# Kernel optimization log

Hardware: AMD Instinct MI355X
Metric: run time of the kernel (lower is better)

Reference implementation:

```python
import jax, jax.numpy as jnp
import numpy as np

C, FF, NH = 128, 2048, 8
B, D, H, W = 1, 16, 16, 16
EPS = 1e-5

def setup_inputs() -> dict:
    key = jax.random.key(0)
    ks = jax.random.split(key, 20)
    s = 0.02
    inp = {
        'x': jax.random.normal(ks[0], (B, C, D, H, W), jnp.float32),
        'Wq': jax.random.normal(ks[1], (C, C), jnp.float32) * s,
        'bq': jnp.zeros((C,), jnp.float32),
        'Wk': jax.random.normal(ks[2], (C, C), jnp.float32) * s,
        'bk': jnp.zeros((C,), jnp.float32),
        'Wv': jax.random.normal(ks[3], (C, C), jnp.float32) * s,
        'bv': jnp.zeros((C,), jnp.float32),
        'Wo': jax.random.normal(ks[4], (C, C), jnp.float32) * s,
        'bo': jnp.zeros((C,), jnp.float32),
        'W1': jax.random.normal(ks[5], (FF, C), jnp.float32) * s,
        'b1': jnp.zeros((FF,), jnp.float32),
        'W2': jax.random.normal(ks[6], (C, FF), jnp.float32) * s,
        'b2': jnp.zeros((C,), jnp.float32),
        'g1': jnp.ones((C,), jnp.float32),
        'be1': jnp.zeros((C,), jnp.float32),
        'g2': jnp.ones((C,), jnp.float32),
        'be2': jnp.zeros((C,), jnp.float32),
    }
    return inp

def _layernorm(t, g, b):
    # normalize over last (channel) dim, biased variance like torch LayerNorm
    m = jnp.mean(t, axis=-1, keepdims=True)
    v = jnp.mean(jnp.square(t - m), axis=-1, keepdims=True)
    return (t - m) * jax.lax.rsqrt(v + EPS) * g + b

def reference(x, Wq, bq, Wk, bk, Wv, bv, Wo, bo, W1, b1, W2, b2, g1, be1, g2, be2):
    b_, c, d, h, w = x.shape
    n = d * h * w
    hd = c // NH
    xf = x.reshape(b_, c, n)  # [B,C,N]
    # 1x1 conv3d == per-voxel linear over channels
    q = jnp.einsum('oc,bcn->bon', Wq, xf) + bq[:, None]
    k = jnp.einsum('oc,bcn->bon', Wk, xf) + bk[:, None]
    v = jnp.einsum('oc,bcn->bon', Wv, xf) + bv[:, None]
    q = q.reshape(b_, NH, hd, n)
    k = k.reshape(b_, NH, hd, n)
    v = v.reshape(b_, NH, hd, n)
    scores = jnp.einsum('bhcd,bhce->bhde', q, k) / (hd ** 0.5)  # [B,NH,N,N]
    probs = jax.nn.softmax(scores, axis=-1)
    attn = jnp.einsum('bhde,bhce->bhcd', probs, v).reshape(b_, c, n)
    attn = jnp.einsum('oc,bcn->bon', Wo, attn) + bo[:, None]
    x1 = xf + attn  # residual (dropout = identity at eval)
    x1 = _layernorm(x1.transpose(0, 2, 1), g1, be1)  # [B,N,C]
    hmid = jax.nn.relu(jnp.einsum('fc,bnc->bnf', W1, x1) + b1)
    ffn = jnp.einsum('cf,bnf->bnc', W2, hmid) + b2
    x2 = _layernorm(x1 + ffn, g2, be2)
    return x2.transpose(0, 2, 1).reshape(b_, c, d, h, w)
```

## Files before the change

### kernel.cpp

```cpp
#include <hip/hip_runtime.h>
#include <hip/hip_bf16.h>

typedef __hip_bfloat16 bf16;
typedef short short8 __attribute__((ext_vector_type(8)));
typedef float f32x4 __attribute__((ext_vector_type(4)));
typedef unsigned int u32x4 __attribute__((ext_vector_type(4)));

#define C_   128
#define N_   4096
#define NH_  8
#define HD_  16
#define FF_  2048
#define SCALE_Q 0.360673760222241f

__device__ __forceinline__ unsigned short f2bf_bits(float f) {
    bf16 h = __float2bfloat16(f);
    return *reinterpret_cast<unsigned short*>(&h);
}
__device__ __forceinline__ unsigned int pack_trunc(float lo, float hi) {
    return __builtin_amdgcn_perm(__float_as_uint(hi), __float_as_uint(lo), 0x07060302u);
}
__device__ __forceinline__ short f2bf_trunc(float f) {
    return (short)(__float_as_uint(f) >> 16);
}
__device__ __forceinline__ float bfs2f(short s) {
    return __uint_as_float(((unsigned int)(unsigned short)s) << 16);
}
__device__ __forceinline__ float fast_exp2(float x) {
    return __builtin_amdgcn_exp2f(x);
}
__device__ __forceinline__ f32x4 mfma16(short8 a, short8 b, f32x4 c) {
    return __builtin_amdgcn_mfma_f32_16x16x32_bf16(a, b, c, 0, 0, 0);
}

__global__ void __launch_bounds__(256) k_prep(
    const float* __restrict__ Wq, const float* __restrict__ Wk,
    const float* __restrict__ Wv, const float* __restrict__ Wo,
    const float* __restrict__ W1, const float* __restrict__ W2,
    const float* __restrict__ x,
    bf16* __restrict__ Wqkvf, bf16* __restrict__ Wof,
    bf16* __restrict__ W1f, bf16* __restrict__ W2f,
    bf16* __restrict__ xTf)
{
    const int i = blockIdx.x * 256 + threadIdx.x;
    if (i < 73728) {
        const float* row;
        bf16* dst;
        int kblk, g;
        if (i < 8192) {
            const int o = i >> 4;
            kblk = (i >> 2) & 3; g = i & 3;
            const int odx = (o < 384) ? o : o - 384;
            row = (o < 128) ? (Wq + o * 128)
                : (o < 256) ? (Wk + (o - 128) * 128)
                : (o < 384) ? (Wv + (o - 256) * 128)
                            : (Wo + (o - 384) * 128);
            bf16* buf = (o < 384) ? Wqkvf : Wof;
            dst = buf + ((((odx >> 4) << 2) + kblk) * 512 + ((g << 4) + (odx & 15)) * 8);
        } else if (i < 40960) {
            const int t = i - 8192, o = t >> 4;
            kblk = (t >> 2) & 3; g = t & 3;
            row = W1 + o * 128;
            dst = W1f + ((((o >> 4) << 2) + kblk) * 512 + ((g << 4) + (o & 15)) * 8);
        } else {
            const int t = i - 40960, o = t >> 8;
            kblk = (t >> 2) & 63; g = t & 3;
            row = W2 + o * 2048;
            dst = W2f + ((((o >> 4) << 6) + kblk) * 512 + ((g << 4) + (o & 15)) * 8);
        }
        const int k0 = kblk * 32 + g * 4;
        const f32x4 lo = *(const f32x4*)(row + k0);
        const f32x4 hi = *(const f32x4*)(row + k0 + 16);
        u32x4 w;
        #pragma unroll
        for (int j = 0; j < 4; ++j)
            w[j] = ((unsigned int)f2bf_bits(hi[j]) << 16) | f2bf_bits(lo[j]);
        *(u32x4*)dst = w;
    } else {
        const int t = i - 73728;
        const int n = t & 4095, g = (t >> 12) & 3, cblk = t >> 14;
        const int c0 = cblk * 32 + g * 4;
        const float* xs = x + (size_t)c0 * 4096 + n;
        u32x4 w;
        #pragma unroll
        for (int j = 0; j < 4; ++j)
            w[j] = ((unsigned int)f2bf_bits(xs[(size_t)(16 + j) * 4096]) << 16)
                 | f2bf_bits(xs[(size_t)j * 4096]);
        bf16* dst = xTf + ((((n >> 4) << 2) + cblk) * 512 + ((g << 4) + (n & 15)) * 8);
        *(u32x4*)dst = w;
    }
}

__global__ void __launch_bounds__(256) k_qkv(
    const bf16* __restrict__ xTf, const bf16* __restrict__ Wqkvf,
    const float* __restrict__ bq, const float* __restrict__ bk, const float* __restrict__ bv,
    bf16* __restrict__ qf, bf16* __restrict__ kf, bf16* __restrict__ vf)
{
    const int tid = threadIdx.x, wave = tid >> 6, lane = tid & 63;
    const int col = lane & 15, quad = lane >> 4;
    const int gw = blockIdx.x * 4 + wave;
    const int rt = gw / 24, ct = gw % 24;
    f32x4 acc = {};
    #pragma unroll
    for (int c = 0; c < 4; ++c) {
        short8 a = *(const short8*)(xTf + ((size_t)(rt * 4 + c) << 9) + lane * 8);
        short8 b = *(const short8*)(Wqkvf + ((size_t)(ct * 4 + c) << 9) + lane * 8);
        acc = mfma16(a, b, acc);
    }
    #pragma unroll
    for (int r = 0; r < 4; ++r) {
        const int m = rt * 16 + quad * 4 + r;
        const int n = ct * 16 + col;
        const float v = acc[r];
        if (n < 128) {
            const int h = n >> 4, ch = n & 15;
            qf[((h << 8) + (m >> 4)) * 256 + (((ch >> 3) << 4) + (m & 15)) * 8 + (ch & 7)] =
                __float2bfloat16((v + bq[n]) * SCALE_Q);
        } else if (n < 256) {
            const int c2 = n - 128, h = c2 >> 4, ch = c2 & 15;
            kf[((h << 8) + (m >> 4)) * 256 + (((ch >> 3) << 4) + (m & 15)) * 8 + (ch & 7)] =
                __float2bfloat16(v + bk[c2]);
        } else {
            const int c2 = n - 256, h = c2 >> 4, ch = c2 & 15;
            const int ko = m & 31;
            const int pos = ((ko & 15) << 1) + (ko >> 4);
            vf[((h << 7) + (m >> 5)) * 512 + (((pos >> 3) << 4) + ch) * 8 + (pos & 7)] =
                __float2bfloat16(v + bv[c2]);
        }
    }
}

__global__ void __launch_bounds__(256)
attn_kernel(const bf16* __restrict__ qf, const bf16* __restrict__ kf,
            const bf16* __restrict__ vf, bf16* __restrict__ af)
{
    __shared__ __align__(16) union {
        unsigned int P[4][2][320];
        float comb[4][64][8];
    } sh;
    const int tid = threadIdx.x, wave = tid >> 6, lane = tid & 63;
    const int col = lane & 15, quad = lane >> 4;
    const int gw = blockIdx.x;
    const int h  = gw >> 8;
    const int tile = gw & 255;
    const f32x4 zero = {};

    short8 aq = {};
    if (quad < 2)
        aq = *(const short8*)(qf + ((size_t)((h << 8) + tile) << 8) + lane * 8);

    const short8 onesb = { (short)0x3F80, (short)0x3F80, (short)0x3F80, (short)0x3F80,
                           (short)0x3F80, (short)0x3F80, (short)0x3F80, (short)0x3F80 };

    f32x4 accO0 = {}, accO1 = {}, accLa = {}, accLb = {};

    const int kbeg = wave << 10;
    unsigned int* P0 = &sh.P[wave][0][0];
    unsigned int* P1 = &sh.P[wave][1][0];

    for (int i = 0; i < 32; i += 2) {
        const int mA = kbeg + (i << 5);
        const int mB = mA + 32;

        short8 bkA0 = {}, bkA1 = {}, bkB0 = {}, bkB1 = {};
        if (quad < 2) {
            const bf16* ka = kf + ((size_t)((h << 8) + (mA >> 4)) << 8) + lane * 8;
            bkA0 = *(const short8*)(ka);
            bkA1 = *(const short8*)(ka + 256);
            bkB0 = *(const short8*)(ka + 512);
            bkB1 = *(const short8*)(ka + 768);
        }
        f32x4 s0 = mfma16(aq, bkA0, zero);
        f32x4 s1 = mfma16(aq, bkA1, zero);
        f32x4 s2 = mfma16(aq, bkB0, zero);
        f32x4 s3 = mfma16(aq, bkB1, zero);
        #pragma unroll
        for (int r = 0; r < 4; ++r) {
            P0[(quad * 4 + r) * 20 + col] = pack_trunc(fast_exp2(s0[r]), fast_exp2(s1[r]));
            P1[(quad * 4 + r) * 20 + col] = pack_trunc(fast_exp2(s2[r]), fast_exp2(s3[r]));
        }
        short8 vA = *(const short8*)(vf + ((size_t)((h << 7) + (mA >> 5)) << 9) + lane * 8);
        short8 vB = *(const short8*)(vf + ((size_t)((h << 7) + (mB >> 5)) << 9) + lane * 8);
        short8 ap0 = *(const short8*)((const short*)P0 + col * 40 + quad * 8);
        accO0 = mfma16(ap0, vA, accO0);
        accLa = mfma16(ap0, onesb, accLa);
        short8 ap1 = *(const short8*)((const short*)P1 + col * 40 + quad * 8);
        accO1 = mfma16(ap1, vB, accO1);
        accLb = mfma16(ap1, onesb, accLb);
    }

    f32x4 accO, accL;
    #pragma unroll
    for (int r = 0; r < 4; ++r) {
        accO[r] = accO0[r] + accO1[r];
        accL[r] = accLa[r] + accLb[r];
    }

    __syncthreads();
    #pragma unroll
    for (int r = 0; r < 4; ++r) {
        sh.comb[wave][lane][r]     = accO[r];
        sh.comb[wave][lane][4 + r] = accL[r];
    }
    __syncthreads();

    if (wave == 0) {
        #pragma unroll
        for (int r = 0; r < 4; ++r) {
            float O = sh.comb[0][lane][r] + sh.comb[1][lane][r]
                    + sh.comb[2][lane][r] + sh.comb[3][lane][r];
            float l = sh.comb[0][lane][4+r] + sh.comb[1][lane][4+r]
                    + sh.comb[2][lane][4+r] + sh.comb[3][lane][4+r];
            const int row16 = quad * 4 + r;
            const int pk = (col << 1) + (h & 1);
            af[((tile << 2) + (h >> 1)) * 512 + (((pk >> 3) << 4) + row16) * 8 + (pk & 7)] =
                __float2bfloat16(O / l);
        }
    }
}

__global__ void __launch_bounds__(512, 2)
k_mega(const bf16* __restrict__ af, const bf16* __restrict__ xTf,
       const bf16* __restrict__ Wof, const bf16* __restrict__ W1f, const bf16* __restrict__ W2f,
       const float* __restrict__ bo, const float* __restrict__ b1, const float* __restrict__ b2,
       const float* __restrict__ g1, const float* __restrict__ be1,
       const float* __restrict__ g2, const float* __restrict__ be2,
       float* __restrict__ out)
{
    __shared__ __align__(16) unsigned int Pb[8][2][320];
    __shared__ float comb[224][64];
    const int tid = threadIdx.x, wave = tid >> 6, lane = tid & 63;
    const int col = lane & 15, quad = lane >> 4;
    const int rt = blockIdx.x, n0 = rt << 4;
    const f32x4 zero = {};

    short8 ao[4], xt[4];
    #pragma unroll
    for (int c = 0; c < 4; ++c) {
        ao[c] = *(const short8*)(af  + ((size_t)(rt * 4 + c) << 9) + lane * 8);
        xt[c] = *(const short8*)(xTf + ((size_t)(rt * 4 + c) << 9) + lane * 8);
    }
    f32x4 d[8];
    #pragma unroll
    for (int t = 0; t < 8; ++t) d[t] = zero;
    #pragma unroll
    for (int t = 0; t < 8; ++t)
        #pragma unroll
        for (int c = 0; c < 4; ++c) {
            short8 b = *(const short8*)(Wof + ((size_t)(t * 4 + c) << 9) + lane * 8);
            d[t] = mfma16(ao[c], b, d[t]);
        }
    #pragma unroll
    for (int t = 0; t < 8; ++t) {
        const float bt = bo[t * 16 + col];
        #pragma unroll
        for (int r = 0; r < 4; ++r) d[t][r] += bt;
    }

    float x1f[4][8];
    #pragma unroll
    for (int c = 0; c < 4; ++c) {
        unsigned int* Pw = &Pb[wave][c & 1][0];
        const short* Ps = (const short*)Pw;
        #pragma unroll
        for (int r = 0; r < 4; ++r)
            Pw[(quad * 4 + r) * 20 + col] = pack_trunc(d[2 * c][r], d[2 * c + 1][r]);
        short8 ar = *(const short8*)(Ps + col * 40 + quad * 8);
        #pragma unroll
        for (int j = 0; j < 8; ++j)
            x1f[c][j] = bfs2f(ar[j]) + bfs2f(xt[c][j]);
    }

    float s = 0.f, ss = 0.f;
    #pragma unroll
    for (int c = 0; c < 4; ++c)
        #pragma unroll
        for (int j = 0; j < 8; ++j) { s += x1f[c][j]; ss += x1f[c][j] * x1f[c][j]; }
    s  += __shfl_xor(s, 16);  s  += __shfl_xor(s, 32);
    ss += __shfl_xor(ss, 16); ss += __shfl_xor(ss, 32);
    const float m1 = s * (1.f / 128.f);
    const float rstd1 = rsqrtf(ss * (1.f / 128.f) - m1 * m1 + 1e-5f);
    short8 aq1[4];
    #pragma unroll
    for (int c = 0; c < 4; ++c)
        #pragma unroll
        for (int j = 0; j < 8; ++j) {
            const int pos = quad * 8 + j;
            const int ko = ((pos & 1) << 4) + (pos >> 1);
            const int ch = c * 32 + ko;
            aq1[c][j] = f2bf_trunc((x1f[c][j] - m1) * rstd1 * g1[ch] + be1[ch]);
        }

    f32x4 ACC[8];
    #pragma unroll
    for (int t = 0; t < 8; ++t) ACC[t] = zero;
    for (int i = 0; i < 8; ++i) {
        const int ffc = (wave << 3) + i;
        f32x4 p0 = zero, p1 = zero;
        #pragma unroll
        for (int c = 0; c < 4; ++c) {
            short8 b = *(const short8*)(W1f + ((size_t)(ffc * 8 + c) << 9) + lane * 8);
            p0 = mfma16(aq1[c], b, p0);
        }
        #pragma unroll
        for (int c = 0; c < 4; ++c) {
            short8 b = *(const short8*)(W1f + ((size_t)(ffc * 8 + 4 + c) << 9) + lane * 8);
            p1 = mfma16(aq1[c], b, p1);
        }
        const float bb0 = b1[ffc * 32 + col], bb1 = b1[ffc * 32 + 16 + col];
        unsigned int* Pw = &Pb[wave][i & 1][0];
        #pragma unroll
        for (int r = 0; r < 4; ++r)
            Pw[(quad * 4 + r) * 20 + col] =
                pack_trunc(fmaxf(p0[r] + bb0, 0.f), fmaxf(p1[r] + bb1, 0.f));
        short8 ah = *(const short8*)((const short*)Pw + col * 40 + quad * 8);
        #pragma unroll
        for (int t = 0; t < 8; ++t) {
            short8 bw = *(const short8*)(W2f + ((size_t)(t * 64 + ffc) << 9) + lane * 8);
            ACC[t] = mfma16(ah, bw, ACC[t]);
        }
    }

    if (wave) {
        #pragma unroll
        for (int t = 0; t < 8; ++t)
            #pragma unroll
            for (int r = 0; r < 4; ++r)
                comb[(wave - 1) * 32 + t * 4 + r][lane] = ACC[t][r];
    }
    __syncthreads();
    if (wave == 0) {
        #pragma unroll
        for (int t = 0; t < 8; ++t)
            #pragma unroll
            for (int r = 0; r < 4; ++r) {
                float acc = ACC[t][r];
                #pragma unroll
                for (int w = 0; w < 7; ++w)
                    acc += comb[w * 32 + t * 4 + r][lane];
                ACC[t][r] = acc;
            }
        short* xb = (short*)&Pb[0][0][0];
        #pragma unroll
        for (int c = 0; c < 4; ++c)
            *(short8*)(xb + (col * 4 + c) * 32 + quad * 8) = aq1[c];
        float t2[8][4];
        #pragma unroll
        for (int t = 0; t < 8; ++t) {
            const int ch = t * 16 + col;
            const int pk = (col << 1) + (t & 1);
            const int c = t >> 1;
            const float bb = b2[ch];
            #pragma unroll
            for (int r = 0; r < 4; ++r)
                t2[t][r] = ACC[t][r] + bb + bfs2f(xb[((quad * 4 + r) * 4 + c) * 32 + pk]);
        }
        #pragma unroll
        for (int r = 0; r < 4; ++r) {
            float S = 0.f, SS = 0.f;
            #pragma unroll
            for (int t = 0; t < 8; ++t) { S += t2[t][r]; SS += t2[t][r] * t2[t][r]; }
            S  += __shfl_xor(S, 1);  S  += __shfl_xor(S, 2);
            S  += __shfl_xor(S, 4);  S  += __shfl_xor(S, 8);
            SS += __shfl_xor(SS, 1); SS += __shfl_xor(SS, 2);
            SS += __shfl_xor(SS, 4); SS += __shfl_xor(SS, 8);
            const float m2 = S * (1.f / 128.f);
            const float rstd2 = rsqrtf(SS * (1.f / 128.f) - m2 * m2 + 1e-5f);
            #pragma unroll
            for (int t = 0; t < 8; ++t) {
                const int ch = t * 16 + col;
                out[(size_t)ch * N_ + n0 + quad * 4 + r] =
                    (t2[t][r] - m2) * rstd2 * g2[ch] + be2[ch];
            }
        }
    }
}

extern "C" void kernel_launch(void* const* d_in, const int* in_sizes, int n_in,
                              void* d_out, int out_size, void* d_ws, size_t ws_size,
                              hipStream_t stream) {
    const float* x   = (const float*)d_in[0];
    const float* Wq  = (const float*)d_in[1];
    const float* bq  = (const float*)d_in[2];
    const float* Wk  = (const float*)d_in[3];
    const float* bk  = (const float*)d_in[4];
    const float* Wv  = (const float*)d_in[5];
    const float* bv  = (const float*)d_in[6];
    const float* Wo  = (const float*)d_in[7];
    const float* bo  = (const float*)d_in[8];
    const float* W1  = (const float*)d_in[9];
    const float* b1  = (const float*)d_in[10];
    const float* W2  = (const float*)d_in[11];
    const float* b2  = (const float*)d_in[12];
    const float* g1  = (const float*)d_in[13];
    const float* be1 = (const float*)d_in[14];
    const float* g2  = (const float*)d_in[15];
    const float* be2 = (const float*)d_in[16];
    float* out = (float*)d_out;

    char* ws = (char*)d_ws;
    bf16* xTf   = (bf16*)(ws + 0);
    bf16* qf    = (bf16*)(ws + 1048576);
    bf16* kf    = (bf16*)(ws + 2097152);
    bf16* vf    = (bf16*)(ws + 3145728);
    bf16* af    = (bf16*)(ws + 4194304);
    bf16* Wqkvf = (bf16*)(ws + 5242880);
    bf16* Wof   = (bf16*)(ws + 5341184);
    bf16* W1f   = (bf16*)(ws + 5373952);
    bf16* W2f   = (bf16*)(ws + 5898240);

    k_prep<<<544, 256, 0, stream>>>(Wq, Wk, Wv, Wo, W1, W2, x, Wqkvf, Wof, W1f, W2f, xTf);
    k_qkv<<<1536, 256, 0, stream>>>(xTf, Wqkvf, bq, bk, bv, qf, kf, vf);
    attn_kernel<<<2048, 256, 0, stream>>>(qf, kf, vf, af);
    k_mega<<<256, 512, 0, stream>>>(af, xTf, Wof, W1f, W2f, bo, b1, b2,
                                    g1, be1, g2, be2, out);
}
```

Before: 143.7 us.

## Process four query tiles per attention block to reuse K/V loads

Each attention block now handles four consecutive 16-row query tiles instead of one, so each K and V fragment loaded from global memory feeds four sets of score and PV MFMAs. The grid shrinks from 2048 to 512 blocks. LDS use rises fourfold for both the P buffers and the combine buffer, and all four waves now do the final normalization, one tile each. The cost is fewer blocks and more registers and LDS per block, which may lower occupancy and latency hiding.

```diff
diff --git a/kernel.cpp b/kernel.cpp
--- a/kernel.cpp
+++ b/kernel.cpp
@@ -135,28 +135,30 @@
             const bf16* __restrict__ vf, bf16* __restrict__ af)
 {
     __shared__ __align__(16) union {
-        unsigned int P[4][2][320];
-        float comb[4][64][8];
+        unsigned int P[4][4][2][320];
+        float comb[4][4][64][8];
     } sh;
     const int tid = threadIdx.x, wave = tid >> 6, lane = tid & 63;
     const int col = lane & 15, quad = lane >> 4;
     const int gw = blockIdx.x;
-    const int h  = gw >> 8;
-    const int tile = gw & 255;
+    const int h  = gw >> 6;
+    const int tile0 = (gw & 63) << 2;
     const f32x4 zero = {};
 
-    short8 aq = {};
-    if (quad < 2)
-        aq = *(const short8*)(qf + ((size_t)((h << 8) + tile) << 8) + lane * 8);
+    short8 aq[4] = {{}, {}, {}, {}};
+    if (quad < 2) {
+        #pragma unroll
+        for (int qt = 0; qt < 4; ++qt)
+            aq[qt] = *(const short8*)(qf + ((size_t)((h << 8) + tile0 + qt) << 8) + lane * 8);
+    }
 
     const short8 onesb = { (short)0x3F80, (short)0x3F80, (short)0x3F80, (short)0x3F80,
                            (short)0x3F80, (short)0x3F80, (short)0x3F80, (short)0x3F80 };
 
-    f32x4 accO0 = {}, accO1 = {}, accLa = {}, accLb = {};
+    f32x4 accO[4] = {{}, {}, {}, {}};
+    f32x4 accL[4] = {{}, {}, {}, {}};
 
     const int kbeg = wave << 10;
-    unsigned int* P0 = &sh.P[wave][0][0];
-    unsigned int* P1 = &sh.P[wave][1][0];
 
     for (int i = 0; i < 32; i += 2) {
         const int mA = kbeg + (i << 5);
@@ -170,47 +172,54 @@
             bkB0 = *(const short8*)(ka + 512);
             bkB1 = *(const short8*)(ka + 768);
         }
-        f32x4 s0 = mfma16(aq, bkA0, zero);
-        f32x4 s1 = mfma16(aq, bkA1, zero);
-        f32x4 s2 = mfma16(aq, bkB0, zero);
-        f32x4 s3 = mfma16(aq, bkB1, zero);
+        const short8 vA = *(const short8*)(vf + ((size_t)((h << 7) + (mA >> 5)) << 9) + lane * 8);
+        const short8 vB = *(const short8*)(vf + ((size_t)((h << 7) + (mB >> 5)) << 9) + lane * 8);
+
+        #pragma unroll
+        for (int qt = 0; qt < 4; ++qt) {
+            f32x4 s0 = mfma16(aq[qt], bkA0, zero);
+            f32x4 s1 = mfma16(aq[qt], bkA1, zero);
+            f32x4 s2 = mfma16(aq[qt], bkB0, zero);
+            f32x4 s3 = mfma16(aq[qt], bkB1, zero);
+            unsigned int* P0 = &sh.P[wave][qt][0][0];
+            unsigned int* P1 = &sh.P[wave][qt][1][0];
+            #pragma unroll
+            for (int r = 0; r < 4; ++r) {
+                P0[(quad * 4 + r) * 20 + col] = pack_trunc(fast_exp2(s0[r]), fast_exp2(s1[r]));
+                P1[(quad * 4 + r) * 20 + col] = pack_trunc(fast_exp2(s2[r]), fast_exp2(s3[r]));
+            }
+        }
+        #pragma unroll
+        for (int qt = 0; qt < 4; ++qt) {
+            const short* Ps0 = (const short*)&sh.P[wave][qt][0][0];
+            const short* Ps1 = (const short*)&sh.P[wave][qt][1][0];
+            short8 ap0 = *(const short8*)(Ps0 + col * 40 + quad * 8);
+            accO[qt] = mfma16(ap0, vA, accO[qt]);
+            accL[qt] = mfma16(ap0, onesb, accL[qt]);
+            short8 ap1 = *(const short8*)(Ps1 + col * 40 + quad * 8);
+            accO[qt] = mfma16(ap1, vB, accO[qt]);
+            accL[qt] = mfma16(ap1, onesb, accL[qt]);
+        }
+    }
+
+    __syncthreads();
+    #pragma unroll
+    for (int qt = 0; qt < 4; ++qt)
         #pragma unroll
         for (int r = 0; r < 4; ++r) {
-            P0[(quad * 4 + r) * 20 + col] = pack_trunc(fast_exp2(s0[r]), fast_exp2(s1[r]));
-            P1[(quad * 4 + r) * 20 + col] = pack_trunc(fast_exp2(s2[r]), fast_exp2(s3[r]));
-        }
-        short8 vA = *(const short8*)(vf + ((size_t)((h << 7) + (mA >> 5)) << 9) + lane * 8);
-        short8 vB = *(const short8*)(vf + ((size_t)((h << 7) + (mB >> 5)) << 9) + lane * 8);
-        short8 ap0 = *(const short8*)((const short*)P0 + col * 40 + quad * 8);
-        accO0 = mfma16(ap0, vA, accO0);
-        accLa = mfma16(ap0, onesb, accLa);
-        short8 ap1 = *(const short8*)((const short*)P1 + col * 40 + quad * 8);
-        accO1 = mfma16(ap1, vB, accO1);
-        accLb = mfma16(ap1, onesb, accLb);
-    }
-
-    f32x4 accO, accL;
-    #pragma unroll
-    for (int r = 0; r < 4; ++r) {
-        accO[r] = accO0[r] + accO1[r];
-        accL[r] = accLa[r] + accLb[r];
-    }
-
+            sh.comb[qt][wave][lane][r]     = accO[qt][r];
+            sh.comb[qt][wave][lane][4 + r] = accL[qt][r];
+        }
     __syncthreads();
-    #pragma unroll
-    for (int r = 0; r < 4; ++r) {
-        sh.comb[wave][lane][r]     = accO[r];
-        sh.comb[wave][lane][4 + r] = accL[r];
-    }
-    __syncthreads();
-
-    if (wave == 0) {
+
+    {
+        const int qt = wave, tile = tile0 + qt;
         #pragma unroll
         for (int r = 0; r < 4; ++r) {
-            float O = sh.comb[0][lane][r] + sh.comb[1][lane][r]
-                    + sh.comb[2][lane][r] + sh.comb[3][lane][r];
-            float l = sh.comb[0][lane][4+r] + sh.comb[1][lane][4+r]
-                    + sh.comb[2][lane][4+r] + sh.comb[3][lane][4+r];
+            float O = sh.comb[qt][0][lane][r] + sh.comb[qt][1][lane][r]
+                    + sh.comb[qt][2][lane][r] + sh.comb[qt][3][lane][r];
+            float l = sh.comb[qt][0][lane][4+r] + sh.comb[qt][1][lane][4+r]
+                    + sh.comb[qt][2][lane][4+r] + sh.comb[qt][3][lane][4+r];
             const int row16 = quad * 4 + r;
             const int pk = (col << 1) + (h & 1);
             af[((tile << 2) + (h >> 1)) * 512 + (((pk >> 3) << 4) + row16) * 8 + (pk & 7)] =
@@ -411,7 +420,7 @@
 
     k_prep<<<544, 256, 0, stream>>>(Wq, Wk, Wv, Wo, W1, W2, x, Wqkvf, Wof, W1f, W2f, xTf);
     k_qkv<<<1536, 256, 0, stream>>>(xTf, Wqkvf, bq, bk, bv, qf, kf, vf);
-    attn_kernel<<<2048, 256, 0, stream>>>(qf, kf, vf, af);
+    attn_kernel<<<512, 256, 0, stream>>>(qf, kf, vf, af);
     k_mega<<<256, 512, 0, stream>>>(af, xTf, Wof, W1f, W2f, bo, b1, b2,
                                     g1, be1, g2, be2, out);
 }
```

Measured after the change: 139.2 us. 1.03x faster.
